# Kernel tuning notes

Measured on AMD Instinct MI355X. Metric: run time of the kernel, lower is better.

Reference implementation:

```python
import jax, jax.numpy as jnp
import numpy as np

EMBED_DIM = 1024
NHEAD = 16
HEAD_DIM = EMBED_DIM // NHEAD  # 64
B, S = 2, 2048


def _rotate_half(x):
    x1, x2 = jnp.split(x, 2, axis=-1)
    return jnp.concatenate([-x2, x1], axis=-1)


def _apply_rope(t, cos, sin):
    # t: (B, H, S, Dh); cos/sin: (S, Dh) broadcast over leading dims
    return t * cos + _rotate_half(t) * sin


def setup_inputs() -> dict:
    key = jax.random.key(0)
    ks = jax.random.split(key, 6)
    x = jax.random.normal(ks[0], (B, S, EMBED_DIM), dtype=jnp.float32)
    # real RoPE tables: theta_i = 10000^(-2i/Dh), duplicated for the two halves
    inv_freq = 1.0 / (10000.0 ** (jnp.arange(0, HEAD_DIM, 2, dtype=jnp.float32) / HEAD_DIM))
    freqs = jnp.outer(jnp.arange(S, dtype=jnp.float32), inv_freq)  # (S, Dh/2)
    emb = jnp.concatenate([freqs, freqs], axis=-1)  # (S, Dh)
    cos = jnp.cos(emb)
    sin = jnp.sin(emb)
    W_in = jax.random.normal(ks[1], (EMBED_DIM, 3 * EMBED_DIM), dtype=jnp.float32) * 0.02
    b_in = jax.random.normal(ks[2], (3 * EMBED_DIM,), dtype=jnp.float32) * 0.02
    W_out = jax.random.normal(ks[3], (EMBED_DIM, EMBED_DIM), dtype=jnp.float32) * 0.02
    b_out = jax.random.normal(ks[4], (EMBED_DIM,), dtype=jnp.float32) * 0.02
    return {"x": x, "cos": cos, "sin": sin, "W_in": W_in, "b_in": b_in,
            "W_out": W_out, "b_out": b_out}


def reference(x, cos, sin, W_in, b_in, W_out, b_out):
    Bs, Ss, D = x.shape
    qkv = x @ W_in + b_in  # (B, S, 3D)
    q, k, v = jnp.split(qkv, 3, axis=-1)
    # (B, S, D) -> (B, H, S, Dh)
    def heads(t):
        return t.reshape(Bs, Ss, NHEAD, HEAD_DIM).transpose(0, 2, 1, 3)
    q, k, v = heads(q), heads(k), heads(v)
    q = _apply_rope(q, cos, sin)
    k = _apply_rope(k, cos, sin)
    scale = 1.0 / jnp.sqrt(jnp.array(HEAD_DIM, dtype=x.dtype))
    scores = jnp.einsum('bhqd,bhkd->bhqk', q, k) * scale
    attn = jax.nn.softmax(scores, axis=-1)
    out = jnp.einsum('bhqk,bhkd->bhqd', attn, v)
    out = out.transpose(0, 2, 1, 3).reshape(Bs, Ss, D)
    return out @ W_out + b_out
```

## Files before the change

kernel.cpp:

```cpp
#include <hip/hip_runtime.h>
#include <hip/hip_bf16.h>

typedef float f32x4 __attribute__((ext_vector_type(4)));
typedef short s16x8 __attribute__((ext_vector_type(8)));

typedef const __attribute__((address_space(1))) unsigned int* as1u;
typedef __attribute__((address_space(3))) unsigned int* as3u;

__device__ __forceinline__ unsigned short f2bf(float f) {
    union { float f; unsigned u; } v; v.f = f;
    unsigned u = v.u;
    u += 0x7fffu + ((u >> 16) & 1u);
    return (unsigned short)(u >> 16);
}

__device__ __forceinline__ void gload16(const void* g, void* l3) {
    __builtin_amdgcn_global_load_lds((as1u)g, (as3u)l3, 16, 0, 0);
}

__device__ __forceinline__ int swzo(int row, int cb) {
    return row * 128 + (cb ^ ((row & 7) << 4));
}

#define LOG2E 1.4426950408889634f
#define QSCALE (0.125f * LOG2E)

__global__ __launch_bounds__(256) void prep_kernel(
    const float* __restrict__ x, unsigned short* __restrict__ xb,
    const float* __restrict__ W_in, unsigned short* __restrict__ Wt_in,
    const float* __restrict__ W_out, unsigned short* __restrict__ Wot)
{
    const int t = threadIdx.x;
    int blk = blockIdx.x;
    if (blk < 2048) {
        size_t i = ((size_t)blk * 256 + t) * 8;
        float4 a = *(const float4*)&x[i];
        float4 b = *(const float4*)&x[i + 4];
        s16x8 p;
        p[0] = (short)f2bf(a.x); p[1] = (short)f2bf(a.y);
        p[2] = (short)f2bf(a.z); p[3] = (short)f2bf(a.w);
        p[4] = (short)f2bf(b.x); p[5] = (short)f2bf(b.y);
        p[6] = (short)f2bf(b.z); p[7] = (short)f2bf(b.w);
        *(s16x8*)&xb[i] = p;
        return;
    }
    const float* W;
    unsigned short* Wt;
    int N;
    if (blk < 2816) { blk -= 2048; W = W_in;  Wt = Wt_in; N = 3072; }
    else            { blk -= 2816; W = W_out; Wt = Wot;   N = 1024; }
    __shared__ alignas(16) short T[64 * 64];
    const int KB = 16;
    const int kb = blk % KB, nb = blk / KB;
#pragma unroll
    for (int pass = 0; pass < 4; ++pass) {
        int k = pass * 16 + (t >> 4);
        int n4 = (t & 15) * 4;
        float4 v = *(const float4*)&W[(size_t)(kb * 64 + k) * N + nb * 64 + n4];
        short4 s4;
        s4.x = (short)f2bf(v.x); s4.y = (short)f2bf(v.y);
        s4.z = (short)f2bf(v.z); s4.w = (short)f2bf(v.w);
        *(short4*)((char*)T + k * 128 + ((n4 * 2) ^ ((k & 7) << 4))) = s4;
    }
    __syncthreads();
#pragma unroll
    for (int pass = 0; pass < 4; ++pass) {
        int n = pass * 16 + (t >> 4);
        int k4 = (t & 15) * 4;
        short4 s4;
        s4.x = *(const short*)((const char*)T + (k4 + 0) * 128 + ((n * 2) ^ (((k4 + 0) & 7) << 4)));
        s4.y = *(const short*)((const char*)T + (k4 + 1) * 128 + ((n * 2) ^ (((k4 + 1) & 7) << 4)));
        s4.z = *(const short*)((const char*)T + (k4 + 2) * 128 + ((n * 2) ^ (((k4 + 2) & 7) << 4)));
        s4.w = *(const short*)((const char*)T + (k4 + 3) * 128 + ((n * 2) ^ (((k4 + 3) & 7) << 4)));
        *(short4*)&Wt[(size_t)(nb * 64 + n) * 1024 + kb * 64 + k4] = s4;
    }
}

__global__ __launch_bounds__(512, 2) void qkv_rope_kernel(
    const unsigned short* __restrict__ xb, const unsigned short* __restrict__ Wt,
    const float* __restrict__ bias, const float* __restrict__ cosb,
    const float* __restrict__ sinb,
    unsigned short* __restrict__ Qb, unsigned short* __restrict__ Kb,
    unsigned short* __restrict__ Vb)
{
    __shared__ alignas(16) short As[2][256 * 64];
    __shared__ alignas(16) short Bs[2][256 * 64];
    const int bid = blockIdx.x;
    const int mb = bid & 15, nb = bid >> 4;
    const int t = threadIdx.x, w = t >> 6, l = t & 63;
    const int g = l >> 4, j = l & 15;
    const int wm = w >> 2, wn = w & 3;
    const int m0 = mb * 256, n0 = nb * 256;

    f32x4 acc[8][4];
#pragma unroll
    for (int mi = 0; mi < 8; ++mi)
#pragma unroll
        for (int ni = 0; ni < 4; ++ni) acc[mi][ni] = (f32x4){0.f, 0.f, 0.f, 0.f};

#pragma unroll
    for (int i = 0; i < 4; ++i) {
        int p = (w * 4 + i) * 1024 + l * 16;
        int r = p >> 7, lb = (p & 127) ^ ((r & 7) << 4);
        gload16(&xb[(size_t)(m0 + r) * 1024 + (lb >> 1)], (char*)As[0] + (w * 4 + i) * 1024);
        gload16(&Wt[(size_t)(n0 + r) * 1024 + (lb >> 1)], (char*)Bs[0] + (w * 4 + i) * 1024);
    }
    asm volatile("s_waitcnt vmcnt(0)" ::: "memory");
    __builtin_amdgcn_s_barrier();

    for (int kti = 0; kti < 16; ++kti) {
        const int cur = kti & 1, nxt = cur ^ 1;
        const int ktn = ((kti + 1) & 15) * 64;

#pragma unroll
        for (int i = 0; i < 4; ++i) {
            int p = (w * 4 + i) * 1024 + l * 16;
            int r = p >> 7, lb = (p & 127) ^ ((r & 7) << 4);
            gload16(&xb[(size_t)(m0 + r) * 1024 + ktn + (lb >> 1)], (char*)As[nxt] + (w * 4 + i) * 1024);
            gload16(&Wt[(size_t)(n0 + r) * 1024 + ktn + (lb >> 1)], (char*)Bs[nxt] + (w * 4 + i) * 1024);
        }
        asm volatile("s_waitcnt vmcnt(8)" ::: "memory");
        __builtin_amdgcn_s_barrier();

#pragma unroll
        for (int kf = 0; kf < 2; ++kf) {
            s16x8 bv[4];
#pragma unroll
            for (int ni = 0; ni < 4; ++ni)
                bv[ni] = *(const s16x8*)((const char*)Bs[cur] + swzo(wn * 64 + ni * 16 + j, kf * 64 + g * 16));
#pragma unroll
            for (int mh = 0; mh < 2; ++mh) {
                s16x8 af[4];
#pragma unroll
                for (int mi = 0; mi < 4; ++mi)
                    af[mi] = *(const s16x8*)((const char*)As[cur] + swzo(wm * 128 + mh * 64 + mi * 16 + j, kf * 64 + g * 16));
                __builtin_amdgcn_s_setprio(1);
#pragma unroll
                for (int mi = 0; mi < 4; ++mi)
#pragma unroll
                    for (int ni = 0; ni < 4; ++ni)
                        acc[mh * 4 + mi][ni] = __builtin_amdgcn_mfma_f32_16x16x32_bf16(af[mi], bv[ni], acc[mh * 4 + mi][ni], 0, 0, 0);
                __builtin_amdgcn_s_setprio(0);
            }
        }
        __builtin_amdgcn_s_barrier();
    }

    const int row0 = m0 + wm * 128;
    const int col0 = n0 + wn * 64;
    const int sec = col0 >> 10;
    const int h = (col0 & 1023) >> 6;

    if (sec < 2) {
        unsigned short* dst = (sec == 0) ? Qb : Kb;
        const float qs = (sec == 0) ? QSCALE : 1.0f;
#pragma unroll
        for (int nt = 0; nt < 2; ++nt) {
            const int d = nt * 16 + j;
            const float b1 = bias[col0 + d];
            const float b2 = bias[col0 + d + 32];
#pragma unroll
            for (int mi = 0; mi < 8; ++mi) {
#pragma unroll
                for (int r = 0; r < 4; ++r) {
                    int row = row0 + mi * 16 + g * 4 + r;
                    int s = row & 2047, bb = row >> 11;
                    float c = cosb[s * 64 + d], sn = sinb[s * 64 + d];
                    float x1 = acc[mi][nt][r] + b1;
                    float x2 = acc[mi][nt + 2][r] + b2;
                    float lo = (x1 * c - x2 * sn) * qs;
                    float hi = (x1 * sn + x2 * c) * qs;
                    size_t base = ((size_t)(bb * 16 + h) * 2048 + s) * 64;
                    dst[base + d] = f2bf(lo);
                    dst[base + d + 32] = f2bf(hi);
                }
            }
        }
    } else {
#pragma unroll
        for (int nt = 0; nt < 4; ++nt) {
            const int d = nt * 16 + j;
            const float bvv = bias[col0 + d];
#pragma unroll
            for (int mi = 0; mi < 8; ++mi) {
#pragma unroll
                for (int r = 0; r < 4; ++r) {
                    int row = row0 + mi * 16 + g * 4 + r;
                    int s = row & 2047, bb = row >> 11;
                    size_t base = ((size_t)(bb * 16 + h) * 2048 + s) * 64;
                    Vb[base + d] = f2bf(acc[mi][nt][r] + bvv);
                }
            }
        }
    }
}

#define NROUND 16
__global__ __launch_bounds__(512, 4) void attn_kernel(
    const unsigned short* __restrict__ Qb, const unsigned short* __restrict__ Kb,
    const unsigned short* __restrict__ Vb, unsigned short* __restrict__ AO)
{
    __shared__ alignas(16) short Ks[2][2 * 64 * 64];
    __shared__ alignas(16) short Vt[2][2 * 64 * 64];
    const int bid = blockIdx.x;
    const int bh = (bid & 7) + ((bid >> 7) << 3);
    const int qt = (bid >> 3) & 15;
    const int t = threadIdx.x, w = t >> 6, l = t & 63;
    const int g = l >> 4, j = l & 15;
    const unsigned short* Qh = Qb + (size_t)bh * 131072;
    const unsigned short* Kh = Kb + (size_t)bh * 131072;
    const unsigned short* Vh = Vb + (size_t)bh * 131072;
    const int q0 = qt * 128 + w * 16;

    s16x8 aq[2];
    aq[0] = *(const s16x8*)&Qh[(size_t)(q0 + j) * 64 + g * 8];
    aq[1] = *(const s16x8*)&Qh[(size_t)(q0 + j) * 64 + 32 + g * 8];

    float lt_ = 0.f;
    f32x4 o[4];
#pragma unroll
    for (int dt = 0; dt < 4; ++dt) o[dt] = (f32x4){0.f, 0.f, 0.f, 0.f};

    const bool vrole = (w < 4);
    const int tv = t & 255;
    const int vk = (tv & 31) * 2;
    const int vd = (tv >> 5) * 8;
    const int kw = (w & 3);

    s16x8 va[2], vb2[2];

    if (vrole) {
#pragma unroll
        for (int s = 0; s < 2; ++s) {
            va[s]  = *(const s16x8*)&Vh[(size_t)(s * 64 + vk) * 64 + vd];
            vb2[s] = *(const s16x8*)&Vh[(size_t)(s * 64 + vk + 1) * 64 + vd];
        }
    } else {
#pragma unroll
        for (int i = 0; i < 4; ++i) {
            int p = (kw * 4 + i) * 1024 + l * 16;
            int s = p >> 13, q = p & 8191;
            int r = q >> 7, lb = (q & 127) ^ ((r & 7) << 4);
            gload16(&Kh[(size_t)(s * 64 + r) * 64 + (lb >> 1)],
                    (char*)Ks[0] + (kw * 4 + i) * 1024);
        }
    }
    asm volatile("s_waitcnt vmcnt(0)" ::: "memory");
    if (vrole) {
#pragma unroll
        for (int s = 0; s < 2; ++s)
#pragma unroll
            for (int dd = 0; dd < 8; ++dd) {
                int d = vd + dd;
                unsigned pkv = (unsigned)(unsigned short)va[s][dd] | ((unsigned)(unsigned short)vb2[s][dd] << 16);
                *(unsigned*)((char*)Vt[0] + s * 8192 + d * 128 + ((vk * 2) ^ ((d & 7) << 4))) = pkv;
            }
    }
    asm volatile("s_waitcnt lgkmcnt(0)" ::: "memory");
    __builtin_amdgcn_s_barrier();

    for (int rr = 0; rr < NROUND; ++rr) {
        const int cur = rr & 1, nxt = cur ^ 1;
        const int kvp = ((rr + 1) & (NROUND - 1)) * 128;

        if (vrole) {
#pragma unroll
            for (int s = 0; s < 2; ++s) {
                va[s]  = *(const s16x8*)&Vh[(size_t)(kvp + s * 64 + vk) * 64 + vd];
                vb2[s] = *(const s16x8*)&Vh[(size_t)(kvp + s * 64 + vk + 1) * 64 + vd];
            }
        } else {
#pragma unroll
            for (int i = 0; i < 4; ++i) {
                int p = (kw * 4 + i) * 1024 + l * 16;
                int s = p >> 13, q = p & 8191;
                int r = q >> 7, lb = (q & 127) ^ ((r & 7) << 4);
                gload16(&Kh[(size_t)(kvp + s * 64 + r) * 64 + (lb >> 1)],
                        (char*)Ks[nxt] + (kw * 4 + i) * 1024);
            }
        }

        f32x4 sc[2][4];
#pragma unroll
        for (int sub = 0; sub < 2; ++sub)
#pragma unroll
            for (int nt = 0; nt < 4; ++nt) sc[sub][nt] = (f32x4){0.f, 0.f, 0.f, 0.f};
        __builtin_amdgcn_s_setprio(1);
#pragma unroll
        for (int sub = 0; sub < 2; ++sub) {
            const char* kbase = (const char*)Ks[cur] + sub * 8192;
#pragma unroll
            for (int kf = 0; kf < 2; ++kf) {
                s16x8 bk[4];
#pragma unroll
                for (int nt = 0; nt < 4; ++nt)
                    bk[nt] = *(const s16x8*)(kbase + swzo(nt * 16 + j, kf * 64 + g * 16));
#pragma unroll
                for (int nt = 0; nt < 4; ++nt)
                    sc[sub][nt] = __builtin_amdgcn_mfma_f32_16x16x32_bf16(bk[nt], aq[kf], sc[sub][nt], 0, 0, 0);
            }
        }
        __builtin_amdgcn_s_setprio(0);

#pragma unroll
        for (int sub = 0; sub < 2; ++sub) {
            const char* vbase = (const char*)Vt[cur] + sub * 8192;

            float rs = 0.f;
#pragma unroll
            for (int nt = 0; nt < 4; ++nt)
#pragma unroll
                for (int r = 0; r < 4; ++r) {
                    sc[sub][nt][r] = __builtin_amdgcn_exp2f(sc[sub][nt][r]);
                    rs += sc[sub][nt][r];
                }
            lt_ += rs;

            unsigned pk[4][2];
#pragma unroll
            for (int nt = 0; nt < 4; ++nt)
#pragma unroll
                for (int s = 0; s < 2; ++s)
                    asm("v_cvt_pk_bf16_f32 %0, %1, %2"
                        : "=v"(pk[nt][s]) : "v"(sc[sub][nt][2 * s]), "v"(sc[sub][nt][2 * s + 1]));

#pragma unroll
            for (int kf = 0; kf < 2; ++kf) {
                unsigned A0 = pk[2 * kf][0], A1 = pk[2 * kf][1];
                unsigned B0 = pk[2 * kf + 1][0], B1 = pk[2 * kf + 1][1];
                asm("v_permlane32_swap_b32 %0, %1" : "+v"(A0), "+v"(B0));
                asm("v_permlane32_swap_b32 %0, %1" : "+v"(A1), "+v"(B1));
                asm("v_permlane16_swap_b32 %0, %1" : "+v"(A0), "+v"(B0));
                asm("v_permlane16_swap_b32 %0, %1" : "+v"(A1), "+v"(B1));
                union { unsigned u[4]; s16x8 v; } fr;
                fr.u[0] = A0;
                fr.u[1] = A1;
                fr.u[2] = B0;
                fr.u[3] = B1;
                __builtin_amdgcn_s_setprio(1);
#pragma unroll
                for (int dt = 0; dt < 4; ++dt) {
                    s16x8 vb = *(const s16x8*)(vbase + swzo(dt * 16 + j, kf * 64 + g * 16));
                    o[dt] = __builtin_amdgcn_mfma_f32_16x16x32_bf16(fr.v, vb, o[dt], 0, 0, 0);
                }
                __builtin_amdgcn_s_setprio(0);
            }
        }

        if (vrole) {
#pragma unroll
            for (int s = 0; s < 2; ++s)
#pragma unroll
                for (int dd = 0; dd < 8; ++dd) {
                    int d = vd + dd;
                    unsigned pkv = (unsigned)(unsigned short)va[s][dd] | ((unsigned)(unsigned short)vb2[s][dd] << 16);
                    *(unsigned*)((char*)Vt[nxt] + s * 8192 + d * 128 + ((vk * 2) ^ ((d & 7) << 4))) = pkv;
                }
        }
        asm volatile("s_waitcnt vmcnt(0) lgkmcnt(0)" ::: "memory");
        __builtin_amdgcn_s_barrier();
    }

    lt_ += __shfl_xor(lt_, 16);
    lt_ += __shfl_xor(lt_, 32);

    const int b = bh >> 4, h = bh & 15;
#pragma unroll
    for (int r = 0; r < 4; ++r) {
        float inv = 1.0f / __shfl(lt_, g * 4 + r);
        int s = q0 + g * 4 + r;
        size_t base = ((size_t)b * 2048 + s) * 1024 + h * 64;
#pragma unroll
        for (int dt = 0; dt < 4; ++dt)
            AO[base + dt * 16 + j] = f2bf(o[dt][r] * inv);
    }
}

__global__ __launch_bounds__(256, 2) void out_gemm_kernel(
    const unsigned short* __restrict__ A, const unsigned short* __restrict__ Wot,
    const float* __restrict__ bias, float* __restrict__ out)
{
    __shared__ alignas(16) short As[2][128 * 64];
    __shared__ alignas(16) short Bs[2][128 * 64];
    const int bid = blockIdx.x;
    const int xcd = bid & 7, ii = bid >> 3;
    const int mb = (xcd & 3) * 8 + (ii & 7);
    const int nb = (xcd >> 2) * 4 + (ii >> 3);
    const int t = threadIdx.x, w = t >> 6, l = t & 63;
    const int g = l >> 4, j = l & 15;
    const int wm = w >> 1, wn = w & 1;
    const int m0 = mb * 128, n0 = nb * 128;

    f32x4 acc[4][4];
#pragma unroll
    for (int mi = 0; mi < 4; ++mi)
#pragma unroll
        for (int ni = 0; ni < 4; ++ni) acc[mi][ni] = (f32x4){0.f, 0.f, 0.f, 0.f};

#pragma unroll
    for (int i = 0; i < 4; ++i) {
        int p = (w * 4 + i) * 1024 + l * 16;
        int r = p >> 7, lb = (p & 127) ^ ((r & 7) << 4);
        gload16(&A[(size_t)(m0 + r) * 1024 + (lb >> 1)], (char*)As[0] + (w * 4 + i) * 1024);
        gload16(&Wot[(size_t)(n0 + r) * 1024 + (lb >> 1)], (char*)Bs[0] + (w * 4 + i) * 1024);
    }
    asm volatile("s_waitcnt vmcnt(0)" ::: "memory");
    __builtin_amdgcn_s_barrier();

    for (int kti = 0; kti < 16; ++kti) {
        const int cur = kti & 1, nxt = cur ^ 1;
        const int ktn = ((kti + 1) & 15) * 64;

#pragma unroll
        for (int i = 0; i < 4; ++i) {
            int p = (w * 4 + i) * 1024 + l * 16;
            int r = p >> 7, lb = (p & 127) ^ ((r & 7) << 4);
            gload16(&A[(size_t)(m0 + r) * 1024 + ktn + (lb >> 1)], (char*)As[nxt] + (w * 4 + i) * 1024);
            gload16(&Wot[(size_t)(n0 + r) * 1024 + ktn + (lb >> 1)], (char*)Bs[nxt] + (w * 4 + i) * 1024);
        }
        asm volatile("s_waitcnt vmcnt(8)" ::: "memory");
        __builtin_amdgcn_s_barrier();

#pragma unroll
        for (int kf = 0; kf < 2; ++kf) {
            s16x8 af[4], bv[4];
#pragma unroll
            for (int mi = 0; mi < 4; ++mi)
                af[mi] = *(const s16x8*)((const char*)As[cur] + swzo(wm * 64 + mi * 16 + j, kf * 64 + g * 16));
#pragma unroll
            for (int ni = 0; ni < 4; ++ni)
                bv[ni] = *(const s16x8*)((const char*)Bs[cur] + swzo(wn * 64 + ni * 16 + j, kf * 64 + g * 16));
            __builtin_amdgcn_s_setprio(1);
#pragma unroll
            for (int mi = 0; mi < 4; ++mi)
#pragma unroll
                for (int ni = 0; ni < 4; ++ni)
                    acc[mi][ni] = __builtin_amdgcn_mfma_f32_16x16x32_bf16(af[mi], bv[ni], acc[mi][ni], 0, 0, 0);
            __builtin_amdgcn_s_setprio(0);
        }
        __builtin_amdgcn_s_barrier();
    }

    const int row0 = m0 + wm * 64;
    const int col0 = n0 + wn * 64;
#pragma unroll
    for (int ni = 0; ni < 4; ++ni) {
        const int col = col0 + ni * 16 + j;
        const float bvv = bias[col];
#pragma unroll
        for (int mi = 0; mi < 4; ++mi)
#pragma unroll
            for (int r = 0; r < 4; ++r) {
                int row = row0 + mi * 16 + g * 4 + r;
                out[(size_t)row * 1024 + col] = acc[mi][ni][r] + bvv;
            }
    }
}

extern "C" void kernel_launch(void* const* d_in, const int* in_sizes, int n_in,
                              void* d_out, int out_size, void* d_ws, size_t ws_size,
                              hipStream_t stream) {
    const float* x     = (const float*)d_in[0];
    const float* cosb  = (const float*)d_in[1];
    const float* sinb  = (const float*)d_in[2];
    const float* W_in  = (const float*)d_in[3];
    const float* b_in  = (const float*)d_in[4];
    const float* W_out = (const float*)d_in[5];
    const float* b_out = (const float*)d_in[6];
    float* out = (float*)d_out;

    const size_t HBUF = 2ull * 16 * 2048 * 64;
    if (ws_size < (4 * HBUF + 1024 * 1024) * sizeof(unsigned short)) return;
    unsigned short* Qb = (unsigned short*)d_ws;
    unsigned short* Kb = Qb + HBUF;
    unsigned short* Vb = Kb + HBUF;
    unsigned short* R  = Vb + HBUF;
    unsigned short* Wt_in = R;
    unsigned short* AO    = R;
    unsigned short* Wot   = R + HBUF;
    unsigned short* xbuf  = (unsigned short*)d_out;

    hipLaunchKernelGGL(prep_kernel, dim3(3072), dim3(256), 0, stream,
                       x, xbuf, W_in, Wt_in, W_out, Wot);
    hipLaunchKernelGGL(qkv_rope_kernel, dim3(192), dim3(512), 0, stream,
                       xbuf, Wt_in, b_in, cosb, sinb, Qb, Kb, Vb);
    hipLaunchKernelGGL(attn_kernel, dim3(512), dim3(512), 0, stream,
                       Qb, Kb, Vb, AO);
    hipLaunchKernelGGL(out_gemm_kernel, dim3(256), dim3(256), 0, stream,
                       AO, Wot, b_out, out);
}
```

Measured before the change: 119.0 us.

## Switch attention MFMAs to 32x32x16 and double query rows per wave

Rewrites the attention inner loop to use 32x32x16 bf16 MFMA tiles. Each wave now handles 32 query rows instead of 16, so each block covers 256 queries and the grid is halved to 256 blocks. The aim is to reuse each K/V tile loaded from LDS across more queries, cutting LDS traffic and instruction count per FLOP, and to drop one permlane stage when re-laying out P. In exchange there are fewer blocks to fill the GPU, more accumulator registers per thread, and the occupancy hint in launch_bounds is removed.

```diff
diff --git a/kernel.cpp b/kernel.cpp
--- a/kernel.cpp
+++ b/kernel.cpp
@@ -2,6 +2,7 @@
 #include <hip/hip_bf16.h>
 
 typedef float f32x4 __attribute__((ext_vector_type(4)));
+typedef float f32x16 __attribute__((ext_vector_type(16)));
 typedef short s16x8 __attribute__((ext_vector_type(8)));
 
 typedef const __attribute__((address_space(1))) unsigned int* as1u;
@@ -196,30 +197,32 @@
 }
 
 #define NROUND 16
-__global__ __launch_bounds__(512, 4) void attn_kernel(
+__global__ __launch_bounds__(512) void attn_kernel(
     const unsigned short* __restrict__ Qb, const unsigned short* __restrict__ Kb,
     const unsigned short* __restrict__ Vb, unsigned short* __restrict__ AO)
 {
     __shared__ alignas(16) short Ks[2][2 * 64 * 64];
     __shared__ alignas(16) short Vt[2][2 * 64 * 64];
     const int bid = blockIdx.x;
-    const int bh = (bid & 7) + ((bid >> 7) << 3);
-    const int qt = (bid >> 3) & 15;
+    const int xcd = bid & 7, idx = bid >> 3;
+    const int bh = xcd + 8 * (idx & 3);
+    const int qt = idx >> 2;
     const int t = threadIdx.x, w = t >> 6, l = t & 63;
-    const int g = l >> 4, j = l & 15;
+    const int lq = l & 31, lh = l >> 5;
     const unsigned short* Qh = Qb + (size_t)bh * 131072;
     const unsigned short* Kh = Kb + (size_t)bh * 131072;
     const unsigned short* Vh = Vb + (size_t)bh * 131072;
-    const int q0 = qt * 128 + w * 16;
-
-    s16x8 aq[2];
-    aq[0] = *(const s16x8*)&Qh[(size_t)(q0 + j) * 64 + g * 8];
-    aq[1] = *(const s16x8*)&Qh[(size_t)(q0 + j) * 64 + 32 + g * 8];
+    const int q0 = qt * 256 + w * 32;
+
+    s16x8 aq[4];
+#pragma unroll
+    for (int ds = 0; ds < 4; ++ds)
+        aq[ds] = *(const s16x8*)&Qh[(size_t)(q0 + lq) * 64 + ds * 16 + lh * 8];
 
     float lt_ = 0.f;
-    f32x4 o[4];
-#pragma unroll
-    for (int dt = 0; dt < 4; ++dt) o[dt] = (f32x4){0.f, 0.f, 0.f, 0.f};
+    f32x16 o[2];
+#pragma unroll
+    for (int i = 0; i < 16; ++i) { o[0][i] = 0.f; o[1][i] = 0.f; }
 
     const bool vrole = (w < 4);
     const int tv = t & 255;
@@ -280,70 +283,58 @@
             }
         }
 
-        f32x4 sc[2][4];
-#pragma unroll
-        for (int sub = 0; sub < 2; ++sub)
-#pragma unroll
-            for (int nt = 0; nt < 4; ++nt) sc[sub][nt] = (f32x4){0.f, 0.f, 0.f, 0.f};
-        __builtin_amdgcn_s_setprio(1);
 #pragma unroll
         for (int sub = 0; sub < 2; ++sub) {
             const char* kbase = (const char*)Ks[cur] + sub * 8192;
-#pragma unroll
-            for (int kf = 0; kf < 2; ++kf) {
-                s16x8 bk[4];
-#pragma unroll
-                for (int nt = 0; nt < 4; ++nt)
-                    bk[nt] = *(const s16x8*)(kbase + swzo(nt * 16 + j, kf * 64 + g * 16));
-#pragma unroll
-                for (int nt = 0; nt < 4; ++nt)
-                    sc[sub][nt] = __builtin_amdgcn_mfma_f32_16x16x32_bf16(bk[nt], aq[kf], sc[sub][nt], 0, 0, 0);
-            }
-        }
-        __builtin_amdgcn_s_setprio(0);
-
-#pragma unroll
-        for (int sub = 0; sub < 2; ++sub) {
             const char* vbase = (const char*)Vt[cur] + sub * 8192;
 
+            f32x16 sc[2];
+#pragma unroll
+            for (int i = 0; i < 16; ++i) { sc[0][i] = 0.f; sc[1][i] = 0.f; }
+            __builtin_amdgcn_s_setprio(1);
+#pragma unroll
+            for (int kh = 0; kh < 2; ++kh)
+#pragma unroll
+                for (int ds = 0; ds < 4; ++ds) {
+                    s16x8 kf = *(const s16x8*)(kbase + swzo(kh * 32 + lq, ds * 32 + lh * 16));
+                    sc[kh] = __builtin_amdgcn_mfma_f32_32x32x16_bf16(kf, aq[ds], sc[kh], 0, 0, 0);
+                }
+            __builtin_amdgcn_s_setprio(0);
+
             float rs = 0.f;
 #pragma unroll
-            for (int nt = 0; nt < 4; ++nt)
-#pragma unroll
-                for (int r = 0; r < 4; ++r) {
-                    sc[sub][nt][r] = __builtin_amdgcn_exp2f(sc[sub][nt][r]);
-                    rs += sc[sub][nt][r];
+            for (int kh = 0; kh < 2; ++kh)
+#pragma unroll
+                for (int r = 0; r < 16; ++r) {
+                    sc[kh][r] = __builtin_amdgcn_exp2f(sc[kh][r]);
+                    rs += sc[kh][r];
                 }
             lt_ += rs;
 
-            unsigned pk[4][2];
-#pragma unroll
-            for (int nt = 0; nt < 4; ++nt)
-#pragma unroll
-                for (int s = 0; s < 2; ++s)
+#pragma unroll
+            for (int kh = 0; kh < 2; ++kh) {
+                unsigned X[8];
+#pragma unroll
+                for (int i = 0; i < 8; ++i)
                     asm("v_cvt_pk_bf16_f32 %0, %1, %2"
-                        : "=v"(pk[nt][s]) : "v"(sc[sub][nt][2 * s]), "v"(sc[sub][nt][2 * s + 1]));
-
-#pragma unroll
-            for (int kf = 0; kf < 2; ++kf) {
-                unsigned A0 = pk[2 * kf][0], A1 = pk[2 * kf][1];
-                unsigned B0 = pk[2 * kf + 1][0], B1 = pk[2 * kf + 1][1];
-                asm("v_permlane32_swap_b32 %0, %1" : "+v"(A0), "+v"(B0));
-                asm("v_permlane32_swap_b32 %0, %1" : "+v"(A1), "+v"(B1));
-                asm("v_permlane16_swap_b32 %0, %1" : "+v"(A0), "+v"(B0));
-                asm("v_permlane16_swap_b32 %0, %1" : "+v"(A1), "+v"(B1));
-                union { unsigned u[4]; s16x8 v; } fr;
-                fr.u[0] = A0;
-                fr.u[1] = A1;
-                fr.u[2] = B0;
-                fr.u[3] = B1;
-                __builtin_amdgcn_s_setprio(1);
-#pragma unroll
-                for (int dt = 0; dt < 4; ++dt) {
-                    s16x8 vb = *(const s16x8*)(vbase + swzo(dt * 16 + j, kf * 64 + g * 16));
-                    o[dt] = __builtin_amdgcn_mfma_f32_16x16x32_bf16(fr.v, vb, o[dt], 0, 0, 0);
-                }
-                __builtin_amdgcn_s_setprio(0);
+                        : "=v"(X[i]) : "v"(sc[kh][2 * i]), "v"(sc[kh][2 * i + 1]));
+#pragma unroll
+                for (int ks = 0; ks < 2; ++ks) {
+                    unsigned a0 = X[ks * 4 + 0], a1 = X[ks * 4 + 1];
+                    unsigned b0 = X[ks * 4 + 2], b1 = X[ks * 4 + 3];
+                    asm("v_permlane32_swap_b32 %0, %1" : "+v"(a0), "+v"(b0));
+                    asm("v_permlane32_swap_b32 %0, %1" : "+v"(a1), "+v"(b1));
+                    union { unsigned u[4]; s16x8 v; } fr;
+                    fr.u[0] = a0; fr.u[1] = a1; fr.u[2] = b0; fr.u[3] = b1;
+                    const int kst = kh * 2 + ks;
+                    __builtin_amdgcn_s_setprio(1);
+#pragma unroll
+                    for (int dh = 0; dh < 2; ++dh) {
+                        s16x8 vf = *(const s16x8*)(vbase + swzo(dh * 32 + lq, kst * 32 + lh * 16));
+                        o[dh] = __builtin_amdgcn_mfma_f32_32x32x16_bf16(fr.v, vf, o[dh], 0, 0, 0);
+                    }
+                    __builtin_amdgcn_s_setprio(0);
+                }
             }
         }
 
@@ -361,18 +352,19 @@
         __builtin_amdgcn_s_barrier();
     }
 
-    lt_ += __shfl_xor(lt_, 16);
     lt_ += __shfl_xor(lt_, 32);
+    float inv = 1.0f / lt_;
 
     const int b = bh >> 4, h = bh & 15;
 #pragma unroll
-    for (int r = 0; r < 4; ++r) {
-        float inv = 1.0f / __shfl(lt_, g * 4 + r);
-        int s = q0 + g * 4 + r;
+    for (int r = 0; r < 16; ++r) {
+        int qrow = (r & 3) + 8 * (r >> 2) + 4 * lh;
+        float iv = __shfl(inv, qrow | (l & 32));
+        int s = q0 + qrow;
         size_t base = ((size_t)b * 2048 + s) * 1024 + h * 64;
 #pragma unroll
-        for (int dt = 0; dt < 4; ++dt)
-            AO[base + dt * 16 + j] = f2bf(o[dt][r] * inv);
+        for (int dh = 0; dh < 2; ++dh)
+            AO[base + dh * 32 + lq] = f2bf(o[dh][r] * iv);
     }
 }
 
@@ -484,7 +476,7 @@
                        x, xbuf, W_in, Wt_in, W_out, Wot);
     hipLaunchKernelGGL(qkv_rope_kernel, dim3(192), dim3(512), 0, stream,
                        xbuf, Wt_in, b_in, cosb, sinb, Qb, Kb, Vb);
-    hipLaunchKernelGGL(attn_kernel, dim3(512), dim3(512), 0, stream,
+    hipLaunchKernelGGL(attn_kernel, dim3(256), dim3(512), 0, stream,
                        Qb, Kb, Vb, AO);
     hipLaunchKernelGGL(out_gemm_kernel, dim3(256), dim3(256), 0, stream,
                        AO, Wot, b_out, out);
```

Result: slower. 121.5 us (+2.1%).
